# Optimization experiments

Hardware: AMD Instinct MI355X
Metric: run time of the kernel (lower is better)

Reference implementation:

```python
import jax, jax.numpy as jnp
import numpy as np

B, S, V = 32, 4096, 128
NSEG = S // 2 + 2  # rising-edge boundaries are at most ceil(S/2), so seg_id <= S//2


def sinusoidal_pe(seq_len, d_model, dtype=jnp.float32):
    pos = jnp.arange(seq_len, dtype=jnp.float32)[:, None]              # [S,1]
    div = jnp.exp(jnp.arange(0, d_model, 2, dtype=jnp.float32) * (-np.log(10000.0) / d_model))
    pe = jnp.zeros((seq_len, d_model), dtype=jnp.float32)
    pe = pe.at[:, 0::2].set(jnp.sin(pos * div))
    pe = pe.at[:, 1::2].set(jnp.cos(pos * div))
    return pe.astype(dtype)


def setup_inputs() -> dict:
    key = jax.random.key(0)
    ks = jax.random.split(key, 8)
    return {
        "bert_output": jax.random.normal(ks[0], (B, S, V), dtype=jnp.float32),
        "startpos": jax.random.uniform(ks[1], (B, S), dtype=jnp.float32),
        "Wq": jax.random.normal(ks[2], (V, V), dtype=jnp.float32) * 0.02,
        "bq": jax.random.normal(ks[3], (V,), dtype=jnp.float32) * 0.02,
        "Wk": jax.random.normal(ks[4], (V, V), dtype=jnp.float32) * 0.02,
        "bk": jax.random.normal(ks[5], (V,), dtype=jnp.float32) * 0.02,
        "Wv": jax.random.normal(ks[6], (V, V), dtype=jnp.float32) * 0.02,
        "bv": jax.random.normal(ks[7], (V,), dtype=jnp.float32) * 0.02,
    }


def reference(bert_output, startpos, Wq, bq, Wk, bk, Wv, bv):
    b, s, v = bert_output.shape
    pe = sinusoidal_pe(s, v, bert_output.dtype)
    # positionembedding2 then positionembedding1 (eval mode -> dropout is identity)
    x1 = bert_output + pe          # what gets concatenated at the end
    xseq = x1 + pe                 # per-row sequence fed to pooling and attention (pe added twice, as in source)

    # Rising-edge segment boundaries: mask[t] = start[t]>=0.5 and (t==0 or start[t-1]<0.5)
    ge = startpos >= 0.5
    prev = jnp.concatenate([jnp.zeros((b, 1), dtype=bool), ge[:, :-1]], axis=1)
    mask = ge & (~prev)                                     # [B,S]
    seg_id = jnp.cumsum(mask.astype(jnp.int32), axis=1)     # inclusive cumsum: token's segment index
    num_time_seq = jnp.sum(mask.astype(jnp.int32), axis=1) + 1

    # Mean-pool xseq per segment (segment_sum over flattened (batch, seg) ids)
    flat_ids = (jnp.arange(b, dtype=jnp.int32)[:, None] * NSEG + seg_id).reshape(-1)
    seg_sum = jax.ops.segment_sum(xseq.reshape(b * s, v), flat_ids, num_segments=b * NSEG)
    seg_cnt = jax.ops.segment_sum(jnp.ones((b * s,), xseq.dtype), flat_ids, num_segments=b * NSEG)
    seg_mean = (seg_sum / jnp.maximum(seg_cnt, 1.0)[:, None]).reshape(b, NSEG, v)

    # AttentionLayer (no softmax): out = (q @ K^T / sqrt(S)) @ V  ==  q @ (K^T V) / sqrt(S)
    q_seg = seg_mean @ Wq.T + bq                             # [B,NSEG,V]
    k = xseq @ Wk.T + bk                                     # [B,S,V]
    vv = xseq @ Wv.T + bv                                    # [B,S,V]
    kv = jnp.einsum("bsv,bsw->bvw", k, vv)                  # [B,V,V]
    q_tok = jnp.take_along_axis(q_seg, seg_id[..., None], axis=1)  # broadcast segment q to tokens [B,S,V]
    attn = jnp.einsum("btv,bvw->btw", q_tok, kv) / np.sqrt(float(s)).astype(np.float32)

    out = jnp.concatenate([attn, x1], axis=-1)               # [B,S,2V]
    return out, num_time_seq
```

## Files before the change

kernel.cpp:

```cpp
#include <hip/hip_runtime.h>
#include <hip/hip_bf16.h>

#define BB 32
#define SS 4096
#define VV 128
#define NSEG 2050
#define OUT_TAIL (BB*SS*2*VV)

#define PE_F      0u
#define SEGID_F   524288u
#define NSEGS_F   655360u
#define WQTA_F    655392u
#define WKA_F     671904u
#define ZT_F      688416u
#define ZB_F      966944u
#define ATT_F     2036000u
#define GPART_F   ATT_F
#define SSUM_F    6234400u
#define SCNT_F    14631200u
#define SGLB_F    14696800u

#define ATT_BYTE    ((size_t)ATT_F*4)
#define ZT_BYTE     ((size_t)ZT_F*4)
#define LDS_MAIN    132624

using bfrag8 = __attribute__((ext_vector_type(8))) short;
using usvec8 = __attribute__((ext_vector_type(8))) unsigned short;
using f32x4  = __attribute__((ext_vector_type(4))) float;

__device__ __forceinline__ unsigned short f2bf(float v){
  unsigned int u = __float_as_uint(v);
  u += 0x7fffu + ((u >> 16) & 1u);
  return (unsigned short)(u >> 16);
}
__device__ __forceinline__ float bf2f(unsigned short h){
  return __uint_as_float(((unsigned int)h) << 16);
}

__global__ __launch_bounds__(1024) void k_init(const float* __restrict__ Wq, const float* __restrict__ bq,
                                               const float* __restrict__ Wk, const float* __restrict__ bk,
                                               const float* __restrict__ sp,
                                               float* __restrict__ ws, float* __restrict__ out){
  int bx = blockIdx.x, tid = threadIdx.x;
  if (bx < 32){
    int b = bx;
    __shared__ int wtot[16];
    const float* row = sp + (size_t)b*SS;
    float4 v4 = *(const float4*)(row + tid*4);
    float pv = (tid == 0) ? 0.f : row[tid*4 - 1];
    bool g0 = v4.x >= 0.5f, g1 = v4.y >= 0.5f, g2 = v4.z >= 0.5f, g3 = v4.w >= 0.5f;
    bool gp = (tid == 0) ? false : (pv >= 0.5f);
    int m0 = (g0 && !gp) ? 1 : 0;
    int m1 = (g1 && !g0) ? 1 : 0;
    int m2 = (g2 && !g1) ? 1 : 0;
    int m3 = (g3 && !g2) ? 1 : 0;
    int c0 = m0, c1 = c0+m1, c2 = c1+m2, c3 = c2+m3;
    int lane = tid & 63, wave = tid >> 6;
    int v = c3;
    #pragma unroll
    for (int off = 1; off < 64; off <<= 1){
      int u = __shfl_up(v, off);
      if (lane >= off) v += u;
    }
    if (lane == 63) wtot[wave] = v;
    __syncthreads();
    if (tid < 16){
      int x = wtot[tid];
      #pragma unroll
      for (int off = 1; off < 16; off <<= 1){
        int u = __shfl_up(x, off);
        if (tid >= off) x += u;
      }
      wtot[tid] = x;
    }
    __syncthreads();
    int woff = (wave == 0) ? 0 : wtot[wave-1];
    int excl = woff + v - c3;
    int4 o; o.x = excl+c0; o.y = excl+c1; o.z = excl+c2; o.w = excl+c3;
    *(int4*)((int*)ws + SEGID_F + (size_t)b*SS + tid*4) = o;
    if (tid == 1023){
      int total = woff + v;
      ((int*)ws)[NSEGS_F + b] = total + 1;
      out[OUT_TAIL + b] = (float)(total + 1);
    }
    return;
  }
  if (bx < 288){
    int gid = (bx - 32)*1024 + tid;
    int t = gid >> 6, i = gid & 63;
    float dv = __expf(-0.14391156831212787f * (float)i);
    float ang = (float)t * dv;
    float s, c;
    __sincosf(ang, &s, &c);
    float2 o; o.x = s; o.y = c;
    ((float2*)(ws + PE_F))[(size_t)t*64 + i] = o;
  } else {
    int gid = (bx - 288)*1024 + tid;
    if (gid < 16384){
      int vv = gid >> 7, a = gid & 127;
      ws[WQTA_F + vv*128 + a] = Wq[a*128 + vv];
    } else if (gid < 16512){
      int a = gid - 16384;
      ws[WQTA_F + 128*128 + a] = bq[a];
    } else if (gid < 32896){
      int e = gid - 16512; int a = e >> 7, i = e & 127;
      ws[WKA_F + a*129 + i] = Wk[a*128 + i];
    } else if (gid < 33024){
      int a = gid - 32896;
      ws[WKA_F + a*129 + 128] = bk[a];
    }
  }
}

__global__ __launch_bounds__(1024) void k_main(const float* __restrict__ bert,
                                               float* __restrict__ ws,
                                               float* __restrict__ out){
  extern __shared__ char smem[];
  float* segacc = (float*)(smem + 65536);
  float* cntacc = (float*)(smem + 65536 + 66048);
  unsigned short* lseg = (unsigned short*)(smem + 65536 + 66048 + 516);

  const int tid = threadIdx.x;
  const int b = blockIdx.y, chunk = blockIdx.x;
  const int fgrp4 = tid & 31, trow = tid >> 5;

  const int* segid = (const int*)ws + SEGID_F + (size_t)b*SS;
  const float* pe = ws + PE_F;

  const int wave = tid >> 6, lane = tid & 63;
  const int mi = wave >> 1, njb = (wave & 1) * 4;
  const int l15 = lane & 15, l4 = lane >> 4;
  f32x4 acc[4];
  #pragma unroll
  for (int q = 0; q < 4; ++q) acc[q] = (f32x4){0.f,0.f,0.f,0.f};
  float sp_part = 0.f;
  const int sf = tid & 127, sgrp = tid >> 7;

  for (int sub = 0; sub < 2; ++sub){
    const int t0 = chunk*512 + sub*256;
    int seg0 = segid[t0];
    if (tid < 256) lseg[tid] = (unsigned short)(segid[t0 + tid] - seg0);
    int nl = segid[t0 + 255] - seg0 + 1;
    for (int idx = tid; idx < nl*32; idx += 1024) ((f32x4*)segacc)[idx] = (f32x4){0.f,0.f,0.f,0.f};
    if (tid < nl) cntacc[tid] = 0.f;
    __syncthreads();

    const int tb = t0 + trow*8;
    const float* bp = bert + ((size_t)(b*SS) + tb)*VV + fgrp4*4;
    const float* pp = pe + (size_t)tb*VV + fgrp4*4;
    float* op = out + ((size_t)(b*SS) + tb)*(2*VV) + VV + fgrp4*4;

    f32x4 racc = (f32x4){0.f,0.f,0.f,0.f};
    unsigned short xb[8][4];
    int cur = lseg[trow*8];
    float runlen = 0.f;
    #pragma unroll
    for (int i = 0; i < 8; ++i){
      int ls = lseg[trow*8 + i];
      if (ls != cur){
        #pragma unroll
        for (int j = 0; j < 4; ++j) unsafeAtomicAdd(&segacc[cur*128 + fgrp4*4 + j], racc[j]);
        if (fgrp4 == 0) unsafeAtomicAdd(&cntacc[cur], runlen);
        racc = (f32x4){0.f,0.f,0.f,0.f}; runlen = 0.f; cur = ls;
      }
      f32x4 bv = __builtin_nontemporal_load((const f32x4*)(bp + i*VV));
      f32x4 pv = *(const f32x4*)(pp + i*VV);
      f32x4 x1 = bv + pv;
      __builtin_nontemporal_store(x1, (f32x4*)(op + i*2*VV));
      f32x4 x = x1 + pv;
      racc += x;
      #pragma unroll
      for (int j = 0; j < 4; ++j) xb[i][j] = f2bf(x[j]);
      runlen += 1.f;
    }
    #pragma unroll
    for (int j = 0; j < 4; ++j) unsafeAtomicAdd(&segacc[cur*128 + fgrp4*4 + j], racc[j]);
    if (fgrp4 == 0) unsafeAtomicAdd(&cntacc[cur], runlen);

    #pragma unroll
    for (int j = 0; j < 4; ++j){
      int f = fgrp4*4 + j;
      int sw = (f ^ (f >> 2)) & 7;
      usvec8 v;
      #pragma unroll
      for (int i = 0; i < 8; ++i) v[i] = xb[i][j];
      *(usvec8*)(smem + f*512 + ((trow ^ sw) << 4)) = v;
    }
    __syncthreads();

    float* srow = ws + SSUM_F + ((size_t)(b*NSEG) + seg0)*128;
    for (int idx = tid; idx < nl*32; idx += 1024){
      int r = idx >> 5, c4 = idx & 31;
      f32x4 v = ((f32x4*)segacc)[idx];
      if (r == 0 || r == nl-1){
        #pragma unroll
        for (int j = 0; j < 4; ++j) unsafeAtomicAdd(&srow[r*128 + c4*4 + j], v[j]);
      } else {
        *(f32x4*)(srow + r*128 + c4*4) = v;
      }
    }
    if (tid < nl){
      float c = cntacc[tid];
      float* cp = ws + SCNT_F + (size_t)b*NSEG + seg0 + tid;
      if (tid == 0 || tid == nl-1) unsafeAtomicAdd(cp, c);
      else *cp = c;
    }
    for (int r = sgrp; r < nl; r += 8) sp_part += segacc[r*128 + sf];

    #pragma unroll
    for (int kk = 0; kk < 8; ++kk){
      int gr = kk*4 + l4;
      int fa = mi*16 + l15;
      bfrag8 aF = *(const bfrag8*)(smem + fa*512 + ((gr ^ ((fa ^ (fa>>2)) & 7)) << 4));
      #pragma unroll
      for (int q = 0; q < 4; ++q){
        int fb = (njb + q)*16 + l15;
        bfrag8 bF = *(const bfrag8*)(smem + fb*512 + ((gr ^ ((fb ^ (fb>>2)) & 7)) << 4));
        acc[q] = __builtin_amdgcn_mfma_f32_16x16x32_bf16(aF, bF, acc[q], 0, 0, 0);
      }
    }
    __syncthreads();
  }

  segacc[tid] = sp_part;
  __syncthreads();
  if (tid < 128){
    float s = 0.f;
    #pragma unroll
    for (int k = 0; k < 8; ++k) s += segacc[tid + 128*k];
    unsafeAtomicAdd(ws + SGLB_F + b*128 + tid, s);
  }

  float* gp = ws + GPART_F + ((size_t)(b*8 + chunk) << 14);
  #pragma unroll
  for (int q = 0; q < 4; ++q){
    #pragma unroll
    for (int r = 0; r < 4; ++r){
      int row = mi*16 + l4*4 + r;
      int col = (njb + q)*16 + l15;
      gp[row*128 + col] = acc[q][r];
    }
  }
}

__global__ __launch_bounds__(256) void k_fused(float* __restrict__ ws,
                                               const float* __restrict__ Wv,
                                               const float* __restrict__ bv){
  __shared__ unsigned short Al[64*136];
  __shared__ unsigned short Bl[129*136];
  __shared__ float svals[128];
  __shared__ float bvv[64];
  int b = blockIdx.x, r0 = blockIdx.y*64, tid = threadIdx.x;
  const float* sg = ws + SGLB_F + (size_t)b*128;
  int wave = tid >> 6, lane = tid & 63, l15 = lane & 15, l4 = lane >> 4;

  {
    const f32x4* gq = (const f32x4*)(ws + GPART_F + ((size_t)(b*8) << 14));
    for (int e = tid; e < 4096; e += 256){
      f32x4 a = (f32x4){0.f,0.f,0.f,0.f};
      #pragma unroll
      for (int c = 0; c < 8; ++c) a += gq[((size_t)c << 12) + e];
      int row = e >> 5, c4 = e & 31;
      unsigned short* dst = &Bl[row*136 + c4*4];
      dst[0]=f2bf(a[0]); dst[1]=f2bf(a[1]); dst[2]=f2bf(a[2]); dst[3]=f2bf(a[3]);
    }
    if (tid < 128) Bl[128*136 + tid] = f2bf(sg[tid]);
  }
  {
    int m = tid >> 2;
    int ks = (tid & 3) * 34;
    int ke = min(128, ks + 34);
    for (int k = ks; k < ke; ++k) Al[m*136 + k] = f2bf(Wv[(size_t)(r0+m)*128 + k]);
  }
  if (tid < 128) svals[tid] = sg[tid];
  if (tid >= 128 && tid < 192) bvv[tid-128] = bv[r0 + tid - 128];
  __syncthreads();

  f32x4 acc[9];

  #pragma unroll
  for (int j = 0; j < 9; ++j) acc[j] = (f32x4){0.f,0.f,0.f,0.f};
  #pragma unroll
  for (int kk = 0; kk < 4; ++kk){
    int k = kk*32 + l4*8;
    bfrag8 aF = *(const bfrag8*)&Al[(wave*16 + l15)*136 + k];
    #pragma unroll
    for (int j = 0; j < 9; ++j){
      bfrag8 bF = *(const bfrag8*)&Bl[(j*16 + l15)*136 + k];
      acc[j] = __builtin_amdgcn_mfma_f32_16x16x32_bf16(aF, bF, acc[j], 0, 0, 0);
    }
  }
  #pragma unroll
  for (int j = 0; j < 9; ++j){
    #pragma unroll
    for (int r = 0; r < 4; ++r){
      int lrow = wave*16 + l4*4 + r;
      int n = j*16 + l15;
      if (n < 129){
        float sx = (n < 128) ? svals[n] : 4096.0f;
        Al[lrow*136 + n] = f2bf(acc[j][r] + bvv[lrow]*sx);
      }
    }
  }
  __syncthreads();

  for (int n = tid >> 1; n < 128; n += 128){
    int ks = (tid & 1) * 65;
    int ke = min(129, ks + 65);
    const float* src = ws + WKA_F + (size_t)n*129;
    for (int k = ks; k < ke; ++k) Bl[n*136 + k] = f2bf(src[k]);
  }
  __syncthreads();

  #pragma unroll
  for (int j = 0; j < 9; ++j) acc[j] = (f32x4){0.f,0.f,0.f,0.f};
  #pragma unroll
  for (int kk = 0; kk < 4; ++kk){
    int k = kk*32 + l4*8;
    bfrag8 aF = *(const bfrag8*)&Al[(wave*16 + l15)*136 + k];
    #pragma unroll
    for (int j = 0; j < 8; ++j){
      bfrag8 bF = *(const bfrag8*)&Bl[(j*16 + l15)*136 + k];
      acc[j] = __builtin_amdgcn_mfma_f32_16x16x32_bf16(aF, bF, acc[j], 0, 0, 0);
    }
  }
  #pragma unroll
  for (int j = 0; j < 8; ++j){
    #pragma unroll
    for (int r = 0; r < 4; ++r){
      int lrow = wave*16 + l4*4 + r;
      int n = j*16 + l15;
      float v = acc[j][r] + bf2f(Al[lrow*136 + 128]) * bf2f(Bl[n*136 + 128]);
      acc[j][r] = v;
    }
  }
  #pragma unroll
  for (int j = 0; j < 8; ++j){
    #pragma unroll
    for (int r = 0; r < 4; ++r){
      int lrow = wave*16 + l4*4 + r;
      int n = j*16 + l15;
      if (n < 128) Al[lrow*136 + n] = f2bf(acc[j][r]);
    }
  }
  __syncthreads();

  for (int n = tid >> 1; n < 129; n += 128){
    int ks = (tid & 1) * 65;
    int ke = min(128, ks + 65);
    const float* src = ws + WQTA_F + (size_t)n*128;
    for (int k = ks; k < ke; ++k) Bl[n*136 + k] = f2bf(src[k]);
  }
  __syncthreads();

  #pragma unroll
  for (int j = 0; j < 9; ++j) acc[j] = (f32x4){0.f,0.f,0.f,0.f};
  #pragma unroll
  for (int kk = 0; kk < 4; ++kk){
    int k = kk*32 + l4*8;
    bfrag8 aF = *(const bfrag8*)&Al[(wave*16 + l15)*136 + k];
    #pragma unroll
    for (int j = 0; j < 9; ++j){
      bfrag8 bF = *(const bfrag8*)&Bl[(j*16 + l15)*136 + k];
      acc[j] = __builtin_amdgcn_mfma_f32_16x16x32_bf16(aF, bF, acc[j], 0, 0, 0);
    }
  }
  unsigned short* zt = (unsigned short*)((char*)ws + ZT_BYTE);
  #pragma unroll
  for (int j = 0; j < 9; ++j){
    #pragma unroll
    for (int r = 0; r < 4; ++r){
      int lrow = wave*16 + l4*4 + r;
      int m = r0 + lrow;
      int n = j*16 + l15;
      float z = acc[j][r] * 0.015625f;
      if (n < 128) zt[(size_t)b*17408 + m*136 + n] = f2bf(z);
      else if (n == 128) ws[ZB_F + (size_t)b*128 + m] = z;
    }
  }
}

__global__ __launch_bounds__(256) void k_attn(float* __restrict__ ws){
  int b = blockIdx.y, g0 = blockIdx.x * 64, tid = threadIdx.x;
  int nseg = ((const int*)ws)[NSEGS_F + b];
  if (g0 >= nseg) return;
  __shared__ unsigned short Albs[64*136];
  __shared__ unsigned short Blbs[128*136];
  __shared__ float zbs[128];
  {
    int row = tid >> 2, part = tid & 3;
    int g = g0 + row;
    float rc = 1.f;
    const float* ssum = ws + SSUM_F + ((size_t)(b*NSEG + g))*128;
    if (g < NSEG){ float c = ws[SCNT_F + (size_t)b*NSEG + g]; rc = 1.f / fmaxf(c, 1.f); }
    #pragma unroll
    for (int j = 0; j < 8; ++j){
      int cix = part*32 + j*4;
      float4 v;
      if (g < NSEG) v = *(const float4*)(ssum + cix);
      else { v.x=0.f; v.y=0.f; v.z=0.f; v.w=0.f; }
      unsigned short* dst = &Albs[row*136 + cix];
      dst[0] = f2bf(v.x*rc); dst[1] = f2bf(v.y*rc); dst[2] = f2bf(v.z*rc); dst[3] = f2bf(v.w*rc);
    }
  }
  {
    const unsigned int* src = (const unsigned int*)((const char*)ws + ZT_BYTE + (size_t)b*34816);
    unsigned int* dst = (unsigned int*)Blbs;
    for (int i = tid; i < 8704; i += 256) dst[i] = src[i];
  }
  if (tid < 128) zbs[tid] = ws[ZB_F + (size_t)b*128 + tid];
  __syncthreads();
  int wave = tid >> 6, lane = tid & 63, l15 = lane & 15, l4 = lane >> 4;
  f32x4 acc[8];
  #pragma unroll
  for (int q = 0; q < 8; ++q) acc[q] = (f32x4){0.f,0.f,0.f,0.f};
  #pragma unroll
  for (int kk = 0; kk < 4; ++kk){
    int k = kk*32 + l4*8;
    bfrag8 aF = *(const bfrag8*)&Albs[(wave*16 + l15)*136 + k];
    #pragma unroll
    for (int q = 0; q < 8; ++q){
      bfrag8 bF = *(const bfrag8*)&Blbs[(q*16 + l15)*136 + k];
      acc[q] = __builtin_amdgcn_mfma_f32_16x16x32_bf16(aF, bF, acc[q], 0, 0, 0);
    }
  }
  unsigned short* att = (unsigned short*)((char*)ws + ATT_BYTE);
  #pragma unroll
  for (int q = 0; q < 8; ++q){
    int w = q*16 + l15;
    float zb = zbs[w];
    #pragma unroll
    for (int r = 0; r < 4; ++r){
      int g = g0 + wave*16 + l4*4 + r;
      if (g < NSEG) att[((size_t)(b*NSEG) + g)*128 + w] = f2bf(acc[q][r] + zb);
    }
  }
}

__global__ __launch_bounds__(256) void k_out(const float* __restrict__ ws,
                                             float* __restrict__ out){
  int b = blockIdx.y, c0 = blockIdx.x * 512, tid = threadIdx.x;
  __shared__ unsigned short lsg[512];
  const int* segid = (const int*)ws + SEGID_F + (size_t)b*SS;
  lsg[tid] = (unsigned short)segid[c0 + tid];
  lsg[tid + 256] = (unsigned short)segid[c0 + tid + 256];
  __syncthreads();
  int fgrp = tid & 31, trow = tid >> 5;
  const unsigned short* att = (const unsigned short*)((const char*)ws + ATT_BYTE);
  #pragma unroll 4
  for (int i = 0; i < 64; ++i){
    int tl = i*8 + trow;
    int g = lsg[tl];
    const unsigned short* ap = att + ((size_t)(b*NSEG) + g)*128 + fgrp*4;
    uint2 raw = *(const uint2*)ap;
    f32x4 o;
    o[0] = bf2f((unsigned short)(raw.x & 0xffffu));
    o[1] = bf2f((unsigned short)(raw.x >> 16));
    o[2] = bf2f((unsigned short)(raw.y & 0xffffu));
    o[3] = bf2f((unsigned short)(raw.y >> 16));
    __builtin_nontemporal_store(o, (f32x4*)(out + ((size_t)(b*SS) + c0 + tl)*(2*VV) + fgrp*4));
  }
}

extern "C" void kernel_launch(void* const* d_in, const int* in_sizes, int n_in,
                              void* d_out, int out_size, void* d_ws, size_t ws_size,
                              hipStream_t stream) {
  const float* bert     = (const float*)d_in[0];
  const float* startpos = (const float*)d_in[1];
  const float* Wq       = (const float*)d_in[2];
  const float* bq       = (const float*)d_in[3];
  const float* Wk       = (const float*)d_in[4];
  const float* bk       = (const float*)d_in[5];
  const float* Wv       = (const float*)d_in[6];
  const float* bv       = (const float*)d_in[7];
  float* out = (float*)d_out;
  float* ws  = (float*)d_ws;

  (void)hipFuncSetAttribute(reinterpret_cast<const void*>(k_main),
                            hipFuncAttributeMaxDynamicSharedMemorySize, LDS_MAIN);

  k_init<<<321, 1024, 0, stream>>>(Wq, bq, Wk, bk, startpos, ws, out);
  k_main<<<dim3(8, 32), 1024, LDS_MAIN, stream>>>(bert, ws, out);
  k_fused<<<dim3(32, 2), 256, 0, stream>>>(ws, Wv, bv);
  k_attn<<<dim3(33, 32), 256, 0, stream>>>(ws);
  k_out<<<dim3(8, 32), 256, 0, stream>>>(ws, out);
}
```

Measured before the change: 266.6 us.

## Fuse per-segment attention output broadcast into k_attn using segment start table

k_init now records each segment's starting token index in a segment-start table. k_attn stages its fp32 attention rows in LDS and writes them straight to the output, looping over each segment's token range. This removes the bf16 intermediate attention buffer and the separate k_out gather kernel. The output stores become scalar 4-byte writes spread over variable-length token ranges, which can leave the store work unevenly balanced across blocks.

```diff
diff --git a/kernel.cpp b/kernel.cpp
--- a/kernel.cpp
+++ b/kernel.cpp
@@ -14,13 +14,11 @@
 #define WKA_F     671904u
 #define ZT_F      688416u
 #define ZB_F      966944u
-#define ATT_F     2036000u
-#define GPART_F   ATT_F
+#define GPART_F   2036000u
 #define SSUM_F    6234400u
 #define SCNT_F    14631200u
 #define SGLB_F    14696800u
-
-#define ATT_BYTE    ((size_t)ATT_F*4)
+#define SEGSTART_F 14700896u
 #define ZT_BYTE     ((size_t)ZT_F*4)
 #define LDS_MAIN    132624
 
@@ -78,8 +76,15 @@
     int excl = woff + v - c3;
     int4 o; o.x = excl+c0; o.y = excl+c1; o.z = excl+c2; o.w = excl+c3;
     *(int4*)((int*)ws + SEGID_F + (size_t)b*SS + tid*4) = o;
+    int* sst = (int*)ws + SEGSTART_F + (size_t)b*(NSEG+1);
+    if (m0) sst[o.x] = tid*4 + 0;
+    if (m1) sst[o.y] = tid*4 + 1;
+    if (m2) sst[o.z] = tid*4 + 2;
+    if (m3) sst[o.w] = tid*4 + 3;
+    if (tid == 0) sst[0] = 0;
+    int total = wtot[15];
+    for (int g = total + 1 + tid; g <= NSEG; g += 1024) sst[g] = SS;
     if (tid == 1023){
-      int total = woff + v;
       ((int*)ws)[NSEGS_F + b] = total + 1;
       out[OUT_TAIL + b] = (float)(total + 1);
     }
@@ -380,13 +385,20 @@
   }
 }
 
-__global__ __launch_bounds__(256) void k_attn(float* __restrict__ ws){
+__global__ __launch_bounds__(256) void k_attn(float* __restrict__ ws, float* __restrict__ out){
   int b = blockIdx.y, g0 = blockIdx.x * 64, tid = threadIdx.x;
   int nseg = ((const int*)ws)[NSEGS_F + b];
   if (g0 >= nseg) return;
   __shared__ unsigned short Albs[64*136];
-  __shared__ unsigned short Blbs[128*136];
+  __shared__ __align__(16) char bufB[128*136*2];
+  unsigned short* Blbs = (unsigned short*)bufB;
+  float* attl = (float*)bufB;
   __shared__ float zbs[128];
+  __shared__ int sstart[65];
+  if (tid < 65){
+    int g = g0 + tid;
+    sstart[tid] = (g <= NSEG) ? ((const int*)ws)[SEGSTART_F + (size_t)b*(NSEG+1) + g] : SS;
+  }
   {
     int row = tid >> 2, part = tid & 3;
     int g = g0 + row;
@@ -424,41 +436,27 @@
       acc[q] = __builtin_amdgcn_mfma_f32_16x16x32_bf16(aF, bF, acc[q], 0, 0, 0);
     }
   }
-  unsigned short* att = (unsigned short*)((char*)ws + ATT_BYTE);
+  __syncthreads();
   #pragma unroll
   for (int q = 0; q < 8; ++q){
     int w = q*16 + l15;
     float zb = zbs[w];
     #pragma unroll
     for (int r = 0; r < 4; ++r){
-      int g = g0 + wave*16 + l4*4 + r;
-      if (g < NSEG) att[((size_t)(b*NSEG) + g)*128 + w] = f2bf(acc[q][r] + zb);
-    }
-  }
-}
-
-__global__ __launch_bounds__(256) void k_out(const float* __restrict__ ws,
-                                             float* __restrict__ out){
-  int b = blockIdx.y, c0 = blockIdx.x * 512, tid = threadIdx.x;
-  __shared__ unsigned short lsg[512];
-  const int* segid = (const int*)ws + SEGID_F + (size_t)b*SS;
-  lsg[tid] = (unsigned short)segid[c0 + tid];
-  lsg[tid + 256] = (unsigned short)segid[c0 + tid + 256];
-  __syncthreads();
-  int fgrp = tid & 31, trow = tid >> 5;
-  const unsigned short* att = (const unsigned short*)((const char*)ws + ATT_BYTE);
-  #pragma unroll 4
-  for (int i = 0; i < 64; ++i){
-    int tl = i*8 + trow;
-    int g = lsg[tl];
-    const unsigned short* ap = att + ((size_t)(b*NSEG) + g)*128 + fgrp*4;
-    uint2 raw = *(const uint2*)ap;
-    f32x4 o;
-    o[0] = bf2f((unsigned short)(raw.x & 0xffffu));
-    o[1] = bf2f((unsigned short)(raw.x >> 16));
-    o[2] = bf2f((unsigned short)(raw.y & 0xffffu));
-    o[3] = bf2f((unsigned short)(raw.y >> 16));
-    __builtin_nontemporal_store(o, (f32x4*)(out + ((size_t)(b*SS) + c0 + tl)*(2*VV) + fgrp*4));
+      int row = wave*16 + l4*4 + r;
+      attl[row*128 + w] = acc[q][r] + zb;
+    }
+  }
+  __syncthreads();
+  int colf = tid & 127, half = tid >> 7;
+  float* ob = out + (size_t)b*SS*(2*VV) + colf;
+  for (int gg = 0; gg < 64; ++gg){
+    int ts = sstart[gg], te = sstart[gg+1];
+    if (ts >= te) continue;
+    float v = attl[gg*128 + colf];
+    for (int t = ts + half; t < te; t += 2){
+      __builtin_nontemporal_store(v, ob + (size_t)t*(2*VV));
+    }
   }
 }
 
@@ -482,6 +480,5 @@
   k_init<<<321, 1024, 0, stream>>>(Wq, bq, Wk, bk, startpos, ws, out);
   k_main<<<dim3(8, 32), 1024, LDS_MAIN, stream>>>(bert, ws, out);
   k_fused<<<dim3(32, 2), 256, 0, stream>>>(ws, Wv, bv);
-  k_attn<<<dim3(33, 32), 256, 0, stream>>>(ws);
-  k_out<<<dim3(8, 32), 256, 0, stream>>>(ws, out);
-}
+  k_attn<<<dim3(33, 32), 256, 0, stream>>>(ws, out);
+}
```

After: 266.1 us. Within noise of the previous version (-0.2%).
